# Optimization experiments

Measured on AMD Instinct MI355X. Metric: run time of the kernel, lower is better.

Reference implementation:

```python
import jax, jax.numpy as jnp
import numpy as np

EPS = 1e-8
NEG = -1e9


def setup_inputs() -> dict:
    key = jax.random.key(0)
    k = jax.random.split(key, 5)
    B, C, T, D = 32, 512, 2000, 128
    return {
        "x": jax.random.normal(k[0], (B, C, T), dtype=jnp.float32),
        "attn_w": jax.random.normal(k[1], (D, 3 * C), dtype=jnp.float32) * 0.02,
        "attn_b": jax.random.normal(k[2], (D,), dtype=jnp.float32) * 0.02,
        "ctx_w": jax.random.normal(k[3], (C, D), dtype=jnp.float32) * 0.02,
        "ctx_b": jax.random.normal(k[4], (C,), dtype=jnp.float32) * 0.02,
        "mask": jnp.ones((B, T), dtype=jnp.int32),
    }


def reference(x, attn_w, attn_b, ctx_w, ctx_b, mask):
    # x: (B, C, T); mask: (B, T) with 1 = valid frame
    m = mask.astype(x.dtype)[:, None, :]                      # (B, 1, T)
    lengths = jnp.sum(m, axis=2, keepdims=True)               # (B, 1, 1)
    mean = jnp.sum(x * m, axis=2, keepdims=True) / lengths    # (B, C, 1)
    var = jnp.sum(jnp.square(x - mean) * m, axis=2, keepdims=True) / lengths
    std = jnp.sqrt(jnp.clip(var, EPS))                        # (B, C, 1)
    # global context: concat [x, mean, std] along channels -> (B, 3C, T)
    T = x.shape[2]
    context = jnp.concatenate(
        [x, jnp.broadcast_to(mean, x.shape), jnp.broadcast_to(std, x.shape)], axis=1
    )
    # two 1x1 convs == channel GEMMs
    alpha = jnp.tanh(jnp.einsum("dc,bct->bdt", attn_w, context) + attn_b[None, :, None])
    alpha = jnp.einsum("cd,bdt->bct", ctx_w, alpha) + ctx_b[None, :, None]  # (B, C, T)
    alpha = jnp.where(m == 0, NEG, alpha)
    alpha = jax.nn.softmax(alpha, axis=2)
    pooled_mean = jnp.sum(alpha * x, axis=2)                  # (B, C)
    pooled_var = jnp.sum(alpha * jnp.square(x - pooled_mean[:, :, None]), axis=2)
    pooled_std = jnp.sqrt(jnp.clip(pooled_var, EPS))
    return jnp.concatenate([pooled_mean, pooled_std], axis=1)  # (B, 2C)
```

## Files before the change

### kernel.cpp

```cpp
#include <hip/hip_runtime.h>
#include <hip/hip_bf16.h>
#include <math.h>

#define EPSF 1e-8f
typedef __attribute__((ext_vector_type(8))) short short8;
typedef __attribute__((ext_vector_type(4))) float f32x4;

__device__ __forceinline__ float wred_sum(float v) {
#pragma unroll
  for (int o = 32; o > 0; o >>= 1) v += __shfl_down(v, o, 64);
  return v;
}

static __device__ __forceinline__ unsigned short f2bf(float f) {
  __hip_bfloat16 h = __float2bfloat16(f);
  return *reinterpret_cast<unsigned short*>(&h);
}
static __device__ __forceinline__ float bf2f(unsigned short u) {
  unsigned int v = ((unsigned int)u) << 16;
  float f;
  __builtin_memcpy(&f, &v, 4);
  return f;
}

__global__ __launch_bounds__(256) void k_zero(float* __restrict__ p, int n4) {
  int i = blockIdx.x * 256 + threadIdx.x;
  if (i < n4)
    *reinterpret_cast<float4*>(p + (size_t)i * 4) = (float4){0.f, 0.f, 0.f, 0.f};
}

__global__ __launch_bounds__(256) void k_convert(
    const float* __restrict__ attn_w, const float* __restrict__ ctx_w,
    unsigned short* __restrict__ awb, unsigned short* __restrict__ cwb, int C, int D) {
  int i = blockIdx.x * 256 + threadIdx.x;
  int DC = D * C;
  if (i < DC) {
    int d = i / C, c = i % C;
    awb[i] = f2bf(attn_w[(size_t)d * 3 * C + c]);
  } else if (i < 2 * DC) {
    int j = i - DC;
    cwb[j] = f2bf(ctx_w[j]);
  }
}

__global__ __launch_bounds__(256) void k_ms_tr(
    const float* __restrict__ x, const int* __restrict__ mask,
    float* __restrict__ sums, unsigned short* __restrict__ xbT, int C, int T) {
  int b = blockIdx.z, c0 = blockIdx.x * 64, t0 = blockIdx.y * 64;
  int tid = threadIdx.x;
  int row = tid >> 2, q = tid & 3;
  __shared__ float Xs[64][65];
  const float* xr = x + ((size_t)b * C + c0 + row) * T;
  const int* mr = mask + (size_t)b * T;
  float s1 = 0.f, s2 = 0.f;

#pragma unroll
  for (int ss = 0; ss < 4; ss++) {
    int cc = q + 4 * ss;
    int t = t0 + cc * 4;
    float4 v;
    float mv[4];
    if (t + 3 < T) {
      v = *reinterpret_cast<const float4*>(&xr[t]);
      int4 mm = *reinterpret_cast<const int4*>(&mr[t]);
      mv[0] = (float)mm.x; mv[1] = (float)mm.y; mv[2] = (float)mm.z; mv[3] = (float)mm.w;
    } else {
      v.x = (t < T) ? xr[t] : 0.f;     mv[0] = (t < T) ? (float)mr[t] : 0.f;
      v.y = (t+1 < T) ? xr[t+1] : 0.f; mv[1] = (t+1 < T) ? (float)mr[t+1] : 0.f;
      v.z = (t+2 < T) ? xr[t+2] : 0.f; mv[2] = (t+2 < T) ? (float)mr[t+2] : 0.f;
      v.w = (t+3 < T) ? xr[t+3] : 0.f; mv[3] = (t+3 < T) ? (float)mr[t+3] : 0.f;
    }
    s1 += mv[0]*v.x + mv[1]*v.y + mv[2]*v.z + mv[3]*v.w;
    s2 += mv[0]*v.x*v.x + mv[1]*v.y*v.y + mv[2]*v.z*v.z + mv[3]*v.w*v.w;
    int tl = cc * 4;
    Xs[row][tl+0] = v.x; Xs[row][tl+1] = v.y; Xs[row][tl+2] = v.z; Xs[row][tl+3] = v.w;
  }
  __syncthreads();
  {
    int trow = tid >> 2;
    int t = t0 + trow;
    if (t < T) {
      unsigned short buf[16];
#pragma unroll
      for (int m = 0; m < 16; m++) buf[m] = f2bf(Xs[q * 16 + m][trow]);
      unsigned short* dst = &xbT[((size_t)b * T + t) * C + c0 + q * 16];
      *reinterpret_cast<short8*>(dst) = *reinterpret_cast<short8*>(&buf[0]);
      *reinterpret_cast<short8*>(dst + 8) = *reinterpret_cast<short8*>(&buf[8]);
    }
  }
  s1 += __shfl_down(s1, 2, 4); s1 += __shfl_down(s1, 1, 4);
  s2 += __shfl_down(s2, 2, 4); s2 += __shfl_down(s2, 1, 4);
  if (q == 0) {
    float* sp = &sums[((size_t)b * C + c0 + row) * 2];
    atomicAdd(sp, s1);
    atomicAdd(sp + 1, s2);
  }
}

__global__ __launch_bounds__(256) void k_ms_fin(
    const float* __restrict__ sums, const int* __restrict__ mask,
    float* __restrict__ mean, float* __restrict__ stdv, int C, int T) {
  int b = blockIdx.x;
  int tid = threadIdx.x;
  const int* mr = mask + (size_t)b * T;
  float sl = 0.f;
  for (int t = tid; t < T; t += 256) sl += (float)mr[t];
  __shared__ float rl[4];
  sl = wred_sum(sl);
  if ((tid & 63) == 0) rl[tid >> 6] = sl;
  __syncthreads();
  float L = fmaxf(rl[0] + rl[1] + rl[2] + rl[3], 1.f);
  for (int c = tid; c < C; c += 256) {
    float s1 = sums[((size_t)b * C + c) * 2];
    float s2 = sums[((size_t)b * C + c) * 2 + 1];
    float mu = s1 / L;
    float var = s2 / L - mu * mu;
    mean[(size_t)b * C + c] = mu;
    stdv[(size_t)b * C + c] = sqrtf(fmaxf(var, EPSF));
  }
}

__global__ __launch_bounds__(256) void k_bias2(
    const float* __restrict__ attn_w, const float* __restrict__ attn_b,
    const float* __restrict__ mean, const float* __restrict__ stdv,
    float* __restrict__ bias2, int C, int D) {
  int bd = blockIdx.x;
  int b = bd / D;
  int d = bd % D;
  const float* wr = attn_w + (size_t)d * 3 * C;
  float s = 0.f;
  for (int c = threadIdx.x; c < C; c += 256)
    s += wr[C + c] * mean[(size_t)b * C + c] + wr[2 * C + c] * stdv[(size_t)b * C + c];
  __shared__ float r[4];
  s = wred_sum(s);
  if ((threadIdx.x & 63) == 0) r[threadIdx.x >> 6] = s;
  __syncthreads();
  if (threadIdx.x == 0) bias2[bd] = attn_b[d] + r[0] + r[1] + r[2] + r[3];
}

__global__ __launch_bounds__(256) void k_gemm1(
    const unsigned short* __restrict__ xbT, const unsigned short* __restrict__ awb,
    const float* __restrict__ bias2, unsigned short* __restrict__ alphaT,
    int C, int T, int D) {
  int b = blockIdx.y;
  int t0 = blockIdx.x * 128;
  int tid = threadIdx.x;
  int w = tid >> 6, lane = tid & 63;
  int wt0 = (w >> 1) * 64, wd0 = (w & 1) * 64;
  int l15 = lane & 15, g = lane >> 4;
  __shared__ unsigned short As[128][72];
  __shared__ unsigned short Bs[128][72];
  f32x4 acc[4][4];
#pragma unroll
  for (int i = 0; i < 4; i++)
#pragma unroll
    for (int j = 0; j < 4; j++) acc[i][j] = (f32x4){0.f, 0.f, 0.f, 0.f};

  int srow = tid >> 1, h = tid & 1;
  bool okA = (t0 + srow) < T;
  size_t rowA = ((size_t)b * T + t0 + srow) * C + h * 32;
  size_t rowB = (size_t)srow * C + h * 32;

  short8 ra[4], rb[4];
#pragma unroll
  for (int qq = 0; qq < 4; qq++) {
    ra[qq] = okA ? *reinterpret_cast<const short8*>(&xbT[rowA + qq * 8]) : (short8){};
    rb[qq] = *reinterpret_cast<const short8*>(&awb[rowB + qq * 8]);
  }

  for (int c0 = 0; c0 < C; c0 += 64) {
    __syncthreads();
#pragma unroll
    for (int qq = 0; qq < 4; qq++) {
      *reinterpret_cast<short8*>(&As[srow][h * 32 + qq * 8]) = ra[qq];
      *reinterpret_cast<short8*>(&Bs[srow][h * 32 + qq * 8]) = rb[qq];
    }
    if (c0 + 64 < C) {
      size_t nA = rowA + c0 + 64, nB = rowB + c0 + 64;
#pragma unroll
      for (int qq = 0; qq < 4; qq++) {
        ra[qq] = okA ? *reinterpret_cast<const short8*>(&xbT[nA + qq * 8]) : (short8){};
        rb[qq] = *reinterpret_cast<const short8*>(&awb[nB + qq * 8]);
      }
    }
    __syncthreads();
#pragma unroll
    for (int ks = 0; ks < 2; ks++) {
      short8 a[4], bb[4];
#pragma unroll
      for (int tf = 0; tf < 4; tf++)
        a[tf] = *reinterpret_cast<const short8*>(&As[wt0 + tf * 16 + l15][ks * 32 + g * 8]);
#pragma unroll
      for (int df = 0; df < 4; df++)
        bb[df] = *reinterpret_cast<const short8*>(&Bs[wd0 + df * 16 + l15][ks * 32 + g * 8]);
#pragma unroll
      for (int tf = 0; tf < 4; tf++)
#pragma unroll
        for (int df = 0; df < 4; df++)
          acc[tf][df] = __builtin_amdgcn_mfma_f32_16x16x32_bf16(a[tf], bb[df], acc[tf][df], 0, 0, 0);
    }
  }
#pragma unroll
  for (int df = 0; df < 4; df++) {
    int d = wd0 + df * 16 + l15;
    float bias = bias2[(size_t)b * D + d];
#pragma unroll
    for (int tf = 0; tf < 4; tf++)
#pragma unroll
      for (int r = 0; r < 4; r++) {
        int t = t0 + wt0 + tf * 16 + g * 4 + r;
        if (t < T)
          alphaT[((size_t)b * T + t) * D + d] = f2bf(tanhf(bias + acc[tf][df][r]));
      }
  }
}

__global__ __launch_bounds__(256) void k_pool2(
    const unsigned short* __restrict__ alphaT, const unsigned short* __restrict__ cwb,
    const unsigned short* __restrict__ xbT, const int* __restrict__ mask,
    float* __restrict__ Sacc, int C, int T, int D) {
  int b = blockIdx.z;
  int c0 = blockIdx.y * 64;
  int ch0 = blockIdx.x * 256;
  int tid = threadIdx.x;
  int w = tid >> 6, lane = tid & 63, l15 = lane & 15, g = lane >> 4;
  __shared__ unsigned short Bl[64][136];
  __shared__ unsigned short Xt[64][72];

  short8 a[4];
#pragma unroll
  for (int ks = 0; ks < 4; ks++)
    a[ks] = *reinterpret_cast<const short8*>(
        &cwb[(size_t)(c0 + w * 16 + l15) * D + ks * 32 + g * 8]);
  int cbase = c0 + w * 16 + g * 4;
  float S0[4] = {0.f, 0.f, 0.f, 0.f};
  float S1[4] = {0.f, 0.f, 0.f, 0.f};
  float S2[4] = {0.f, 0.f, 0.f, 0.f};

  const int* mr = mask + (size_t)b * T;
  int srow = tid >> 2, sq = tid & 3;

  int rem = T - ch0;
  int ntt = rem >= 256 ? 4 : (rem + 63) >> 6;

  short8 pa0, pa1, pa2, pa3, px0, px1;
  {
    int trow = ch0 + srow;
    pa0 = pa1 = pa2 = pa3 = px0 = px1 = (short8){};
    if (trow < T) {
      const unsigned short* sa = &alphaT[((size_t)b * T + trow) * D + sq * 32];
      pa0 = *reinterpret_cast<const short8*>(sa);
      pa1 = *reinterpret_cast<const short8*>(sa + 8);
      pa2 = *reinterpret_cast<const short8*>(sa + 16);
      pa3 = *reinterpret_cast<const short8*>(sa + 24);
      const unsigned short* sx = &xbT[((size_t)b * T + trow) * C + c0 + sq * 16];
      px0 = *reinterpret_cast<const short8*>(sx);
      px1 = *reinterpret_cast<const short8*>(sx + 8);
    }
  }

  for (int tt = 0; tt < ntt; tt++) {
    int t0 = ch0 + tt * 64;
    __syncthreads();
    *reinterpret_cast<short8*>(&Bl[srow][sq * 32]) = pa0;
    *reinterpret_cast<short8*>(&Bl[srow][sq * 32 + 8]) = pa1;
    *reinterpret_cast<short8*>(&Bl[srow][sq * 32 + 16]) = pa2;
    *reinterpret_cast<short8*>(&Bl[srow][sq * 32 + 24]) = pa3;
    *reinterpret_cast<short8*>(&Xt[srow][sq * 16]) = px0;
    *reinterpret_cast<short8*>(&Xt[srow][sq * 16 + 8]) = px1;
    if (tt + 1 < ntt) {
      int trow = t0 + 64 + srow;
      pa0 = pa1 = pa2 = pa3 = px0 = px1 = (short8){};
      if (trow < T) {
        const unsigned short* sa = &alphaT[((size_t)b * T + trow) * D + sq * 32];
        pa0 = *reinterpret_cast<const short8*>(sa);
        pa1 = *reinterpret_cast<const short8*>(sa + 8);
        pa2 = *reinterpret_cast<const short8*>(sa + 16);
        pa3 = *reinterpret_cast<const short8*>(sa + 24);
        const unsigned short* sx = &xbT[((size_t)b * T + trow) * C + c0 + sq * 16];
        px0 = *reinterpret_cast<const short8*>(sx);
        px1 = *reinterpret_cast<const short8*>(sx + 8);
      }
    }
    __syncthreads();
#pragma unroll
    for (int tf = 0; tf < 4; tf++) {
      f32x4 p = (f32x4){0.f, 0.f, 0.f, 0.f};
#pragma unroll
      for (int ks = 0; ks < 4; ks++) {
        short8 bb = *reinterpret_cast<const short8*>(&Bl[tf * 16 + l15][ks * 32 + g * 8]);
        p = __builtin_amdgcn_mfma_f32_16x16x32_bf16(a[ks], bb, p, 0, 0, 0);
      }
      int t = t0 + tf * 16 + l15;
      bool valid = (t < T) && (mr[t < T ? t : 0] != 0);
#pragma unroll
      for (int r = 0; r < 4; r++) {
        float e = valid ? __expf(p[r]) : 0.f;
        float xv = bf2f(Xt[tf * 16 + l15][w * 16 + g * 4 + r]);
        S0[r] += e; S1[r] += e * xv; S2[r] += e * xv * xv;
      }
    }
  }

#pragma unroll
  for (int r = 0; r < 4; r++) {
#pragma unroll
    for (int o = 1; o < 16; o <<= 1) {
      S0[r] += __shfl_xor(S0[r], o, 16);
      S1[r] += __shfl_xor(S1[r], o, 16);
      S2[r] += __shfl_xor(S2[r], o, 16);
    }
  }
  if (l15 == 0) {
#pragma unroll
    for (int r = 0; r < 4; r++) {
      float* sp = &Sacc[((size_t)b * C + cbase + r) * 3];
      atomicAdd(sp, S0[r]);
      atomicAdd(sp + 1, S1[r]);
      atomicAdd(sp + 2, S2[r]);
    }
  }
}

__global__ __launch_bounds__(256) void k_out(
    const float* __restrict__ Sacc, float* __restrict__ out, int C) {
  int b = blockIdx.x;
  for (int c = threadIdx.x; c < C; c += 256) {
    float S0 = Sacc[((size_t)b * C + c) * 3];
    float S1 = Sacc[((size_t)b * C + c) * 3 + 1];
    float S2 = Sacc[((size_t)b * C + c) * 3 + 2];
    float pm = S1 / S0;
    float var = S2 / S0 - pm * pm;
    out[(size_t)b * 2 * C + c] = pm;
    out[(size_t)b * 2 * C + C + c] = sqrtf(fmaxf(var, EPSF));
  }
}

extern "C" void kernel_launch(void* const* d_in, const int* in_sizes, int n_in,
                              void* d_out, int out_size, void* d_ws, size_t ws_size,
                              hipStream_t stream) {
  const float* x = (const float*)d_in[0];
  const float* attn_w = (const float*)d_in[1];
  const float* attn_b = (const float*)d_in[2];
  const float* ctx_w = (const float*)d_in[3];
  const int* mask = (const int*)d_in[5];
  float* out = (float*)d_out;

  int D = in_sizes[2];
  int C = in_sizes[4];
  int B = out_size / (2 * C);
  int T = in_sizes[5] / B;

  unsigned short* awb = (unsigned short*)d_ws;
  unsigned short* cwb = awb + (size_t)D * C;
  float* mean = (float*)(cwb + (size_t)C * D);
  float* stdv = mean + (size_t)B * C;
  float* bias2 = stdv + (size_t)B * C;
  float* sums = bias2 + (size_t)B * D;
  float* Sacc = sums + (size_t)B * C * 2;
  unsigned short* xbT = (unsigned short*)(Sacc + (size_t)B * C * 3);
  unsigned short* alphaT = xbT + (size_t)B * T * C;

  int nzero4 = (B * C * 5 + 3) / 4;
  k_zero<<<(nzero4 + 255) / 256, 256, 0, stream>>>(sums, nzero4);
  k_convert<<<(2 * D * C + 255) / 256, 256, 0, stream>>>(attn_w, ctx_w, awb, cwb, C, D);
  k_ms_tr<<<dim3(C / 64, (T + 63) / 64, B), 256, 0, stream>>>(x, mask, sums, xbT, C, T);
  k_ms_fin<<<B, 256, 0, stream>>>(sums, mask, mean, stdv, C, T);
  k_bias2<<<B * D, 256, 0, stream>>>(attn_w, attn_b, mean, stdv, bias2, C, D);
  k_gemm1<<<dim3((T + 127) / 128, B), 256, 0, stream>>>(xbT, awb, bias2, alphaT, C, T, D);
  k_pool2<<<dim3((T + 255) / 256, C / 64, B), 256, 0, stream>>>(
      alphaT, cwb, xbT, mask, Sacc, C, T, D);
  k_out<<<B, 256, 0, stream>>>(Sacc, out, C);
}
```

Baseline: 144.6 us.

## Load pool MFMA operands directly from global memory, dropping LDS staging

The pooling kernel no longer stages alpha and x tiles through shared memory with double-buffered register prefetch and barriers. Each wave now reads its MFMA B operands and x values straight from global memory and iterates over 16-row time slices with a partial unroll. This removes the LDS writes, LDS reads and __syncthreads, but the four waves of a block now each fetch the same alpha rows separately and lose the explicit prefetch pipelining. Out-of-range time indices are clamped to the last valid row rather than zero-filled, and those rows are masked out.

```diff
diff --git a/kernel.cpp b/kernel.cpp
--- a/kernel.cpp
+++ b/kernel.cpp
@@ -4,6 +4,7 @@
 
 #define EPSF 1e-8f
 typedef __attribute__((ext_vector_type(8))) short short8;
+typedef __attribute__((ext_vector_type(4))) short s4v;
 typedef __attribute__((ext_vector_type(4))) float f32x4;
 
 __device__ __forceinline__ float wred_sum(float v) {
@@ -224,8 +225,6 @@
   int ch0 = blockIdx.x * 256;
   int tid = threadIdx.x;
   int w = tid >> 6, lane = tid & 63, l15 = lane & 15, g = lane >> 4;
-  __shared__ unsigned short Bl[64][136];
-  __shared__ unsigned short Xt[64][72];
 
   short8 a[4];
 #pragma unroll
@@ -238,67 +237,26 @@
   float S2[4] = {0.f, 0.f, 0.f, 0.f};
 
   const int* mr = mask + (size_t)b * T;
-  int srow = tid >> 2, sq = tid & 3;
-
-  int rem = T - ch0;
-  int ntt = rem >= 256 ? 4 : (rem + 63) >> 6;
-
-  short8 pa0, pa1, pa2, pa3, px0, px1;
-  {
-    int trow = ch0 + srow;
-    pa0 = pa1 = pa2 = pa3 = px0 = px1 = (short8){};
-    if (trow < T) {
-      const unsigned short* sa = &alphaT[((size_t)b * T + trow) * D + sq * 32];
-      pa0 = *reinterpret_cast<const short8*>(sa);
-      pa1 = *reinterpret_cast<const short8*>(sa + 8);
-      pa2 = *reinterpret_cast<const short8*>(sa + 16);
-      pa3 = *reinterpret_cast<const short8*>(sa + 24);
-      const unsigned short* sx = &xbT[((size_t)b * T + trow) * C + c0 + sq * 16];
-      px0 = *reinterpret_cast<const short8*>(sx);
-      px1 = *reinterpret_cast<const short8*>(sx + 8);
-    }
-  }
-
-  for (int tt = 0; tt < ntt; tt++) {
-    int t0 = ch0 + tt * 64;
-    __syncthreads();
-    *reinterpret_cast<short8*>(&Bl[srow][sq * 32]) = pa0;
-    *reinterpret_cast<short8*>(&Bl[srow][sq * 32 + 8]) = pa1;
-    *reinterpret_cast<short8*>(&Bl[srow][sq * 32 + 16]) = pa2;
-    *reinterpret_cast<short8*>(&Bl[srow][sq * 32 + 24]) = pa3;
-    *reinterpret_cast<short8*>(&Xt[srow][sq * 16]) = px0;
-    *reinterpret_cast<short8*>(&Xt[srow][sq * 16 + 8]) = px1;
-    if (tt + 1 < ntt) {
-      int trow = t0 + 64 + srow;
-      pa0 = pa1 = pa2 = pa3 = px0 = px1 = (short8){};
-      if (trow < T) {
-        const unsigned short* sa = &alphaT[((size_t)b * T + trow) * D + sq * 32];
-        pa0 = *reinterpret_cast<const short8*>(sa);
-        pa1 = *reinterpret_cast<const short8*>(sa + 8);
-        pa2 = *reinterpret_cast<const short8*>(sa + 16);
-        pa3 = *reinterpret_cast<const short8*>(sa + 24);
-        const unsigned short* sx = &xbT[((size_t)b * T + trow) * C + c0 + sq * 16];
-        px0 = *reinterpret_cast<const short8*>(sx);
-        px1 = *reinterpret_cast<const short8*>(sx + 8);
-      }
-    }
-    __syncthreads();
-#pragma unroll
-    for (int tf = 0; tf < 4; tf++) {
-      f32x4 p = (f32x4){0.f, 0.f, 0.f, 0.f};
-#pragma unroll
-      for (int ks = 0; ks < 4; ks++) {
-        short8 bb = *reinterpret_cast<const short8*>(&Bl[tf * 16 + l15][ks * 32 + g * 8]);
-        p = __builtin_amdgcn_mfma_f32_16x16x32_bf16(a[ks], bb, p, 0, 0, 0);
-      }
-      int t = t0 + tf * 16 + l15;
-      bool valid = (t < T) && (mr[t < T ? t : 0] != 0);
-#pragma unroll
-      for (int r = 0; r < 4; r++) {
-        float e = valid ? __expf(p[r]) : 0.f;
-        float xv = bf2f(Xt[tf * 16 + l15][w * 16 + g * 4 + r]);
-        S0[r] += e; S1[r] += e * xv; S2[r] += e * xv * xv;
-      }
+
+#pragma unroll 4
+  for (int tf = 0; tf < 16; tf++) {
+    if (ch0 + tf * 16 >= T) break;
+    int t = ch0 + tf * 16 + l15;
+    int tc = t < T ? t : T - 1;
+    const unsigned short* ar = &alphaT[((size_t)b * T + tc) * D];
+    f32x4 p = (f32x4){0.f, 0.f, 0.f, 0.f};
+#pragma unroll
+    for (int ks = 0; ks < 4; ks++) {
+      short8 bb = *reinterpret_cast<const short8*>(&ar[ks * 32 + g * 8]);
+      p = __builtin_amdgcn_mfma_f32_16x16x32_bf16(a[ks], bb, p, 0, 0, 0);
+    }
+    bool valid = (t < T) && (mr[tc] != 0);
+    s4v xv4 = *reinterpret_cast<const s4v*>(&xbT[((size_t)b * T + tc) * C + cbase]);
+#pragma unroll
+    for (int r = 0; r < 4; r++) {
+      float e = valid ? __expf(p[r]) : 0.f;
+      float xv = bf2f((unsigned short)xv4[r]);
+      S0[r] += e; S1[r] += e * xv; S2[r] += e * xv * xv;
     }
   }
 
```

Result: slower. 185.9 us (+28.5%).
